# Performance work log

Measured on AMD Instinct MI355X. Metric: run time of the kernel, lower is better.

The kernel has to match this reference:

```python
import jax, jax.numpy as jnp
import numpy as np

B, T, C = 4, 2048, 1024
NH = 16
HD = C // NH

def setup_inputs() -> dict:
    key = jax.random.key(0)
    k1, k2, k3 = jax.random.split(key, 3)
    x = jax.random.normal(k1, (B, T, C), dtype=jnp.float32)
    w_attn = jax.random.normal(k2, (C, 3 * C), dtype=jnp.float32) * (1.0 / np.sqrt(C))
    w_proj = jax.random.normal(k3, (C, C), dtype=jnp.float32) * (1.0 / np.sqrt(C))
    return {"x": x, "w_attn": w_attn, "w_proj": w_proj}

def reference(x, w_attn, w_proj):
    b, t, c = x.shape
    qkv = x @ w_attn  # [B,T,3C]
    q, k, v = jnp.split(qkv, 3, axis=-1)
    # [B,T,C] -> [B,NH,T,HD]
    def heads(a):
        return a.reshape(b, t, NH, HD).transpose(0, 2, 1, 3)
    q, k, v = heads(q), heads(k), heads(v)
    scale = 1.0 / np.sqrt(HD)
    att = jnp.einsum('bhqd,bhkd->bhqk', q, k) * scale  # materialized TxT scores
    causal = jnp.tril(jnp.ones((t, t), dtype=bool))
    att = jnp.where(causal, att, -jnp.inf)
    att = jax.nn.softmax(att, axis=-1)
    y = jnp.einsum('bhqk,bhkd->bhqd', att, v)
    y = y.transpose(0, 2, 1, 3).reshape(b, t, c)
    return y @ w_proj
```

## Files before the change

kernel.cpp:

```cpp
#include <hip/hip_runtime.h>

typedef unsigned short u16;
typedef short bf16x8 __attribute__((ext_vector_type(8)));
typedef float f32x4 __attribute__((ext_vector_type(4)));
typedef float f32x16 __attribute__((ext_vector_type(16)));

#define B_  4
#define T_  2048
#define C_  1024
#define NH_ 16
#define HD_ 64

__device__ __forceinline__ void gload16(const u16* g, u16* lds) {
  __builtin_amdgcn_global_load_lds(
      (const __attribute__((address_space(1))) void*)g,
      (__attribute__((address_space(3))) void*)lds, 16, 0, 0);
}

__device__ __forceinline__ u16 f2bf(float f) {
  union { float f; unsigned u; } x; x.f = f;
  unsigned r = x.u + 0x7fffu + ((x.u >> 16) & 1u);
  return (u16)(r >> 16);
}

__device__ __forceinline__ float max3f(float a, float b, float c) {
  return fmaxf(fmaxf(a, b), c);
}

#define PSWAP(a, b) asm("v_permlane32_swap_b32 %0, %1" : "+v"(a), "+v"(b))

__global__ __launch_bounds__(256) void convert_x(const float* __restrict__ in,
                                                 u16* __restrict__ out) {
  int i = (blockIdx.x * 256 + threadIdx.x) * 8;
  float4 a = *(const float4*)(in + i);
  float4 b = *(const float4*)(in + i + 4);
  u16 t[8] = {f2bf(a.x), f2bf(a.y), f2bf(a.z), f2bf(a.w),
              f2bf(b.x), f2bf(b.y), f2bf(b.z), f2bf(b.w)};
  *(uint4*)(out + i) = *(const uint4*)t;
}

__global__ __launch_bounds__(256) void transpose_w(const float* __restrict__ in,
                                                   u16* __restrict__ out,
                                                   int R, int Cc) {
  int r0 = blockIdx.x * 64, c0 = blockIdx.y * 64;
  __shared__ __attribute__((aligned(16))) u16 tile[64][72];
  int tid = threadIdx.x;
#pragma unroll
  for (int it = 0; it < 4; ++it) {
    int chunk = it * 256 + tid;
    int row = chunk >> 4, c4 = chunk & 15;
    float4 v = *(const float4*)(in + (size_t)(r0 + row) * Cc + c0 + c4 * 4);
    tile[row][c4 * 4 + 0] = f2bf(v.x);
    tile[row][c4 * 4 + 1] = f2bf(v.y);
    tile[row][c4 * 4 + 2] = f2bf(v.z);
    tile[row][c4 * 4 + 3] = f2bf(v.w);
  }
  __syncthreads();
#pragma unroll
  for (int it = 0; it < 2; ++it) {
    int chunk = it * 256 + tid;
    int row = chunk >> 3, c8 = chunk & 7;
    uint4 v; u16* tv = (u16*)&v;
#pragma unroll
    for (int k = 0; k < 8; ++k) tv[k] = tile[c8 * 8 + k][row];
    *(uint4*)(out + (size_t)(c0 + row) * R + r0 + c8 * 8) = v;
  }
}

__device__ __forceinline__ void gemm_bt_tile(const u16* __restrict__ A,
                                             const u16* __restrict__ Bt,
                                             int Kdim, int m0, int n0,
                                             u16* sA, u16* sB, f32x4 acc[4][4]) {
  int tid = threadIdx.x;
  int w = tid >> 6, l = tid & 63, li = l & 15, quad = l >> 4;
  int wm = (w >> 1) * 64, wn = (w & 1) * 64;
  f32x4 zero = {0.f, 0.f, 0.f, 0.f};
#pragma unroll
  for (int i = 0; i < 4; ++i)
#pragma unroll
    for (int j = 0; j < 4; ++j) acc[i][j] = zero;

  for (int k0 = 0; k0 < Kdim; k0 += 32) {
#pragma unroll
    for (int r = 0; r < 2; ++r) {
      int chunk = r * 256 + tid;
      int row = chunk >> 2, c8 = chunk & 3;
      gload16(A  + (size_t)(m0 + row) * Kdim + k0 + c8 * 8, sA + chunk * 8);
      gload16(Bt + (size_t)(n0 + row) * Kdim + k0 + c8 * 8, sB + chunk * 8);
    }
    __syncthreads();
    bf16x8 af[4], bfr[4];
#pragma unroll
    for (int i = 0; i < 4; ++i)
      af[i] = *(const bf16x8*)(sA + (wm + i * 16 + li) * 32 + quad * 8);
#pragma unroll
    for (int j = 0; j < 4; ++j)
      bfr[j] = *(const bf16x8*)(sB + (wn + j * 16 + li) * 32 + quad * 8);
#pragma unroll
    for (int i = 0; i < 4; ++i)
#pragma unroll
      for (int j = 0; j < 4; ++j)
        acc[i][j] = __builtin_amdgcn_mfma_f32_16x16x32_bf16(af[i], bfr[j], acc[i][j], 0, 0, 0);
    __syncthreads();
  }
}

__global__ __launch_bounds__(256) void gemm_qkv(const u16* __restrict__ X,
                                                const u16* __restrict__ WT,
                                                u16* __restrict__ Qb,
                                                u16* __restrict__ Kb,
                                                u16* __restrict__ Vt) {
  __shared__ __attribute__((aligned(16))) u16 sA[128 * 32];
  __shared__ __attribute__((aligned(16))) u16 sB[128 * 32];
  f32x4 acc[4][4];
  int m0 = blockIdx.x * 128, n0 = blockIdx.y * 128;
  gemm_bt_tile(X, WT, C_, m0, n0, sA, sB, acc);

  int tid = threadIdx.x;
  int w = tid >> 6, l = tid & 63, li = l & 15, quad = l >> 4;
  int wm = (w >> 1) * 64, wn = (w & 1) * 64;
#pragma unroll
  for (int i = 0; i < 4; ++i)
#pragma unroll
    for (int j = 0; j < 4; ++j) {
      int n = n0 + wn + j * 16 + li;
      int which = n >> 10, cc = n & (C_ - 1);
      int h = cc >> 6, d = cc & (HD_ - 1);
      int mb = m0 + wm + i * 16 + quad * 4;
      int b = mb >> 11, t0 = mb & (T_ - 1);
      if (which == 2) {
        u16 tv[4] = {f2bf(acc[i][j][0]), f2bf(acc[i][j][1]),
                     f2bf(acc[i][j][2]), f2bf(acc[i][j][3])};
        *(uint2*)(Vt + ((size_t)(b * NH_ + h) * HD_ + d) * T_ + t0) = *(const uint2*)tv;
      } else {
        u16* dst = (which == 0) ? Qb : Kb;
#pragma unroll
        for (int r = 0; r < 4; ++r)
          dst[((size_t)(b * NH_ + h) * T_ + t0 + r) * HD_ + d] = f2bf(acc[i][j][r]);
      }
    }
}

__global__ __launch_bounds__(256) void gemm_proj(const u16* __restrict__ Y,
                                                 const u16* __restrict__ WT,
                                                 float* __restrict__ Out) {
  __shared__ __attribute__((aligned(16))) u16 sA[128 * 32];
  __shared__ __attribute__((aligned(16))) u16 sB[128 * 32];
  f32x4 acc[4][4];
  int m0 = blockIdx.x * 128, n0 = blockIdx.y * 128;
  gemm_bt_tile(Y, WT, C_, m0, n0, sA, sB, acc);

  int tid = threadIdx.x;
  int w = tid >> 6, l = tid & 63, li = l & 15, quad = l >> 4;
  int wm = (w >> 1) * 64, wn = (w & 1) * 64;
#pragma unroll
  for (int i = 0; i < 4; ++i)
#pragma unroll
    for (int j = 0; j < 4; ++j)
#pragma unroll
      for (int r = 0; r < 4; ++r) {
        int m = m0 + wm + i * 16 + quad * 4 + r;
        int n = n0 + wn + j * 16 + li;
        Out[(size_t)m * C_ + n] = acc[i][j][r];
      }
}

__global__ __launch_bounds__(256, 2) void attn_k(const u16* __restrict__ Q,
                                                 const u16* __restrict__ K,
                                                 const u16* __restrict__ Vt,
                                                 u16* __restrict__ Y) {
  int bh = blockIdx.x;
  int qt = 15 - (int)blockIdx.y;
  int tid = threadIdx.x;
  int w = tid >> 6, l = tid & 63;
  int l31 = l & 31, hi = l >> 5;
  int qb = qt * 128 + w * 32;
  int qg = qb + l31;

  __shared__ __attribute__((aligned(16))) u16 sK[2][64 * 64];
  __shared__ __attribute__((aligned(16))) u16 sV[2][64 * 64];

  const u16* kbase = K + (size_t)bh * T_ * HD_;
  const u16* vbase = Vt + (size_t)bh * HD_ * T_;

  bf16x8 qf[4];
  {
    const u16* qp = Q + ((size_t)bh * T_ + qg) * HD_ + hi * 8;
#pragma unroll
    for (int c = 0; c < 4; ++c) qf[c] = *(const bf16x8*)(qp + c * 16);
  }

  f32x16 o[2];
#pragma unroll
  for (int dt = 0; dt < 2; ++dt)
#pragma unroll
    for (int r = 0; r < 16; ++r) o[dt][r] = 0.f;
  float mrow = -1e30f, lsum = 0.f;
  const float csc = 0.125f * 1.44269504088896f;

  int nkv = 2 * qt + 2;

  int koff[2], voff[2], ldst[2];
  {
    int r0 = tid >> 3, c0_ = tid & 7;
#pragma unroll
    for (int rr = 0; rr < 2; ++rr) {
      int row = rr * 32 + r0;
      int cs = (c0_ ^ (row & 7)) * 8;
      koff[rr] = row * HD_ + cs;
      voff[rr] = row * T_ + cs;
      ldst[rr] = (rr * 256 + tid) * 8;
    }
  }
  const u16* kst = kbase;
  const u16* vst = vbase;
#define STAGE(buf)                                        \
  {                                                       \
    gload16(kst + koff[0], sK[buf] + ldst[0]);            \
    gload16(vst + voff[0], sV[buf] + ldst[0]);            \
    gload16(kst + koff[1], sK[buf] + ldst[1]);            \
    gload16(vst + voff[1], sV[buf] + ldst[1]);            \
    kst += 64 * HD_; vst += 64;                           \
  }

  STAGE(0);
  __syncthreads();

  int cur = 0;
  for (int kvt = 0; kvt < nkv; ++kvt) {
    int kv0 = kvt * 64;
    if (kvt + 1 < nkv) STAGE(cur ^ 1);

    bool aq = (kv0 <= qb + 31);
    bool a1 = (kv0 + 32 <= qb + 31);
    if (aq) {
      bf16x8 kf0[4], kf1[4];
#pragma unroll
      for (int c = 0; c < 4; ++c) {
        int row = l31;
        int c16 = (2 * c + hi) ^ (row & 7);
        kf0[c] = *(const bf16x8*)(sK[cur] + row * 64 + c16 * 8);
      }
      if (a1) {
#pragma unroll
        for (int c = 0; c < 4; ++c) {
          int row = 32 + l31;
          int c16 = (2 * c + hi) ^ (row & 7);
          kf1[c] = *(const bf16x8*)(sK[cur] + row * 64 + c16 * 8);
        }
      }

      f32x16 st0, st1;
#pragma unroll
      for (int r = 0; r < 16; ++r) { st0[r] = 0.f; st1[r] = 0.f; }
      __builtin_amdgcn_s_setprio(1);
#pragma unroll
      for (int c = 0; c < 4; ++c)
        st0 = __builtin_amdgcn_mfma_f32_32x32x16_bf16(kf0[c], qf[c], st0, 0, 0, 0);
      if (a1) {
#pragma unroll
        for (int c = 0; c < 4; ++c)
          st1 = __builtin_amdgcn_mfma_f32_32x32x16_bf16(kf1[c], qf[c], st1, 0, 0, 0);
      }
      __builtin_amdgcn_s_setprio(0);

      if (kv0 + 63 > qb) {
#pragma unroll
        for (int r = 0; r < 16; ++r) {
          int kvg = kv0 + (r & 3) + 8 * (r >> 2) + 4 * hi;
          if (kvg > qg) st0[r] = -1e30f;
          if (a1 && kvg + 32 > qg) st1[r] = -1e30f;
        }
      }

      float ml = max3f(st0[0], st0[1], st0[2]);
#pragma unroll
      for (int r = 3; r < 15; r += 2) ml = max3f(ml, st0[r], st0[r + 1]);
      ml = fmaxf(ml, st0[15]);
      if (a1) {
#pragma unroll
        for (int r = 0; r < 16; r += 2) ml = max3f(ml, st1[r], st1[r + 1]);
      }
      float mt = fmaxf(ml, __shfl_xor(ml, 32));
      float g = (mt - mrow) * csc;
      if (!__all(g <= 8.0f)) {
        float mnew = fmaxf(mrow, mt);
        float alpha = exp2f((mrow - mnew) * csc);
        mrow = mnew;
        lsum *= alpha;
#pragma unroll
        for (int r = 0; r < 16; ++r) {
          int qlr = (r & 3) + 8 * (r >> 2) + 4 * hi;
          float ar = __shfl(alpha, qlr);
          o[0][r] *= ar;
          o[1][r] *= ar;
        }
      }

      float mc = mrow * csc;
      float ls = 0.f;
#pragma unroll
      for (int r = 0; r < 16; ++r) {
        float p = exp2f(__builtin_fmaf(st0[r], csc, -mc));
        ls += p; st0[r] = p;
      }
      if (a1) {
#pragma unroll
        for (int r = 0; r < 16; ++r) {
          float p = exp2f(__builtin_fmaf(st1[r], csc, -mc));
          ls += p; st1[r] = p;
        }
      }
      lsum += ls;

      union { unsigned uu[16]; bf16x8 v[4]; } pu;
#pragma unroll
      for (int k = 0; k < 8; ++k)
        asm("v_cvt_pk_bf16_f32 %0, %1, %2"
            : "=v"(pu.uu[k]) : "v"(st0[2 * k]), "v"(st0[2 * k + 1]));
      if (a1) {
#pragma unroll
        for (int k = 0; k < 8; ++k)
          asm("v_cvt_pk_bf16_f32 %0, %1, %2"
              : "=v"(pu.uu[8 + k]) : "v"(st1[2 * k]), "v"(st1[2 * k + 1]));
      }
#pragma unroll
      for (int h2 = 0; h2 < 2; ++h2) {
        PSWAP(pu.uu[4 * h2 + 0], pu.uu[4 * h2 + 2]);
        PSWAP(pu.uu[4 * h2 + 1], pu.uu[4 * h2 + 3]);
      }
      if (a1) {
#pragma unroll
        for (int h2 = 0; h2 < 2; ++h2) {
          PSWAP(pu.uu[8 + 4 * h2 + 0], pu.uu[8 + 4 * h2 + 2]);
          PSWAP(pu.uu[8 + 4 * h2 + 1], pu.uu[8 + 4 * h2 + 3]);
        }
      }

      __builtin_amdgcn_s_setprio(1);
#pragma unroll
      for (int dt = 0; dt < 2; ++dt) {
        bf16x8 vf[4];
#pragma unroll
        for (int c = 0; c < 4; ++c) {
          int row = 32 * dt + l31;
          int c16 = (2 * c + hi) ^ (row & 7);
          vf[c] = *(const bf16x8*)(sV[cur] + row * 64 + c16 * 8);
        }
#pragma unroll
        for (int c = 0; c < 4; ++c) {
          if (c >= 2 && !a1) continue;
          o[dt] = __builtin_amdgcn_mfma_f32_32x32x16_bf16(pu.v[c], vf[c], o[dt], 0, 0, 0);
        }
      }
      __builtin_amdgcn_s_setprio(0);
    }

    __syncthreads();
    cur ^= 1;
  }

  int b = bh >> 4, h = bh & (NH_ - 1);
  float lt = lsum + __shfl_xor(lsum, 32);
  float rv = 1.0f / fmaxf(lt, 1e-20f);
#pragma unroll
  for (int r = 0; r < 16; ++r) {
    int qlr = (r & 3) + 8 * (r >> 2) + 4 * hi;
    float rr = __shfl(rv, qlr);
    int qq = qb + qlr;
    size_t base = ((size_t)b * T_ + qq) * C_ + h * HD_;
    Y[base + l31]      = f2bf(o[0][r] * rr);
    Y[base + 32 + l31] = f2bf(o[1][r] * rr);
  }
#undef STAGE
}

extern "C" void kernel_launch(void* const* d_in, const int* in_sizes, int n_in,
                              void* d_out, int out_size, void* d_ws, size_t ws_size,
                              hipStream_t stream) {
  (void)in_sizes; (void)n_in; (void)out_size; (void)ws_size;
  const float* x      = (const float*)d_in[0];
  const float* w_attn = (const float*)d_in[1];
  const float* w_proj = (const float*)d_in[2];
  float* out = (float*)d_out;

  const size_t NTOK = (size_t)B_ * T_ * C_;
  u16* watT   = (u16*)d_ws;
  u16* wprojT = watT   + (size_t)3 * C_ * C_;
  u16* xbf    = wprojT + (size_t)C_ * C_;
  u16* qb     = xbf  + NTOK;
  u16* kb     = qb   + NTOK;
  u16* vtb    = kb   + NTOK;
  u16* yb     = xbf;

  transpose_w<<<dim3(16, 48), 256, 0, stream>>>(w_attn, watT, C_, 3 * C_);
  transpose_w<<<dim3(16, 16), 256, 0, stream>>>(w_proj, wprojT, C_, C_);
  convert_x<<<dim3(4096), 256, 0, stream>>>(x, xbf);
  gemm_qkv<<<dim3(64, 24), 256, 0, stream>>>(xbf, watT, qb, kb, vtb);
  attn_k<<<dim3(64, 16), 256, 0, stream>>>(qb, kb, vtb, yb);
  gemm_proj<<<dim3(64, 8), 256, 0, stream>>>(yb, wprojT, out);
}
```

Baseline: 251.6 us.

## Triple-buffer GEMM mainloop with swizzled LDS and larger 128x256 tiles

```diff
diff --git a/kernel.cpp b/kernel.cpp
--- a/kernel.cpp
+++ b/kernel.cpp
@@ -67,58 +67,101 @@
   }
 }
 
-__device__ __forceinline__ void gemm_bt_tile(const u16* __restrict__ A,
-                                             const u16* __restrict__ Bt,
-                                             int Kdim, int m0, int n0,
-                                             u16* sA, u16* sB, f32x4 acc[4][4]) {
+__device__ __forceinline__ void gemm_mainloop(const u16* __restrict__ A,
+                                              const u16* __restrict__ Bt,
+                                              int m0, int n0,
+                                              u16* sA0, u16* sA1, u16* sA2,
+                                              u16* sB0, u16* sB1, u16* sB2,
+                                              f32x4 acc[4][4]) {
   int tid = threadIdx.x;
   int w = tid >> 6, l = tid & 63, li = l & 15, quad = l >> 4;
-  int wm = (w >> 1) * 64, wn = (w & 1) * 64;
+  int wr = w >> 2, wc = w & 3;
+
   f32x4 zero = {0.f, 0.f, 0.f, 0.f};
 #pragma unroll
-  for (int i = 0; i < 4; ++i)
-#pragma unroll
-    for (int j = 0; j < 4; ++j) acc[i][j] = zero;
-
-  for (int k0 = 0; k0 < Kdim; k0 += 32) {
-#pragma unroll
-    for (int r = 0; r < 2; ++r) {
-      int chunk = r * 256 + tid;
-      int row = chunk >> 2, c8 = chunk & 3;
-      gload16(A  + (size_t)(m0 + row) * Kdim + k0 + c8 * 8, sA + chunk * 8);
-      gload16(Bt + (size_t)(n0 + row) * Kdim + k0 + c8 * 8, sB + chunk * 8);
+  for (int m = 0; m < 4; ++m)
+#pragma unroll
+    for (int n = 0; n < 4; ++n) acc[m][n] = zero;
+
+  int srow = tid >> 3;
+  int sc = (tid & 7) ^ (srow & 7);
+  const u16* aS0 = A + (size_t)(m0 + srow) * C_ + sc * 8;
+  const u16* aS1 = A + (size_t)(m0 + 64 + srow) * C_ + sc * 8;
+  const u16* bS0 = Bt + (size_t)(n0 + srow) * C_ + sc * 8;
+  const u16* bS1 = Bt + (size_t)(n0 + 64 + srow) * C_ + sc * 8;
+  const u16* bS2 = Bt + (size_t)(n0 + 128 + srow) * C_ + sc * 8;
+  const u16* bS3 = Bt + (size_t)(n0 + 192 + srow) * C_ + sc * 8;
+  int ldOff = tid * 8;
+
+#define STAGE6(sa, sb)                                   \
+  {                                                      \
+    gload16(aS0, (sa) + ldOff);                          \
+    gload16(aS1, (sa) + 4096 + ldOff);                   \
+    gload16(bS0, (sb) + ldOff);                          \
+    gload16(bS1, (sb) + 4096 + ldOff);                   \
+    gload16(bS2, (sb) + 8192 + ldOff);                   \
+    gload16(bS3, (sb) + 12288 + ldOff);                  \
+    aS0 += 64; aS1 += 64;                                \
+    bS0 += 64; bS1 += 64; bS2 += 64; bS3 += 64;          \
+  }
+
+  STAGE6(sA0, sB0);
+  STAGE6(sA1, sB1);
+  asm volatile("s_waitcnt vmcnt(6)" ::: "memory");
+  __builtin_amdgcn_s_barrier();
+
+  u16 *aC = sA0, *aN = sA1, *aSt = sA2;
+  u16 *bC = sB0, *bN = sB1, *bSt = sB2;
+
+  int xr = li & 7;
+  int aRow = (wr * 64 + li) * 64;
+  int bRow = (wc * 64 + li) * 64;
+  int ck0 = (quad ^ xr) * 8;
+  int ck1 = ((4 + quad) ^ xr) * 8;
+
+  for (int kt = 0; kt < 16; ++kt) {
+    STAGE6(aSt, bSt);
+    bf16x8 aF0[4], aF1[4], bF0[4], bF1[4];
+#pragma unroll
+    for (int m = 0; m < 4; ++m) {
+      aF0[m] = *(const bf16x8*)(aC + aRow + m * 1024 + ck0);
+      aF1[m] = *(const bf16x8*)(aC + aRow + m * 1024 + ck1);
     }
-    __syncthreads();
-    bf16x8 af[4], bfr[4];
-#pragma unroll
-    for (int i = 0; i < 4; ++i)
-      af[i] = *(const bf16x8*)(sA + (wm + i * 16 + li) * 32 + quad * 8);
-#pragma unroll
-    for (int j = 0; j < 4; ++j)
-      bfr[j] = *(const bf16x8*)(sB + (wn + j * 16 + li) * 32 + quad * 8);
-#pragma unroll
-    for (int i = 0; i < 4; ++i)
-#pragma unroll
-      for (int j = 0; j < 4; ++j)
-        acc[i][j] = __builtin_amdgcn_mfma_f32_16x16x32_bf16(af[i], bfr[j], acc[i][j], 0, 0, 0);
-    __syncthreads();
-  }
-}
-
-__global__ __launch_bounds__(256) void gemm_qkv(const u16* __restrict__ X,
-                                                const u16* __restrict__ WT,
-                                                u16* __restrict__ Qb,
-                                                u16* __restrict__ Kb,
-                                                u16* __restrict__ Vt) {
-  __shared__ __attribute__((aligned(16))) u16 sA[128 * 32];
-  __shared__ __attribute__((aligned(16))) u16 sB[128 * 32];
+#pragma unroll
+    for (int n = 0; n < 4; ++n) {
+      bF0[n] = *(const bf16x8*)(bC + bRow + n * 1024 + ck0);
+      bF1[n] = *(const bf16x8*)(bC + bRow + n * 1024 + ck1);
+    }
+#pragma unroll
+    for (int m = 0; m < 4; ++m)
+#pragma unroll
+      for (int n = 0; n < 4; ++n) {
+        acc[m][n] = __builtin_amdgcn_mfma_f32_16x16x32_bf16(aF0[m], bF0[n], acc[m][n], 0, 0, 0);
+        acc[m][n] = __builtin_amdgcn_mfma_f32_16x16x32_bf16(aF1[m], bF1[n], acc[m][n], 0, 0, 0);
+      }
+    asm volatile("s_waitcnt vmcnt(6)" ::: "memory");
+    __builtin_amdgcn_s_barrier();
+    u16* t;
+    t = aC; aC = aN; aN = aSt; aSt = t;
+    t = bC; bC = bN; bN = bSt; bSt = t;
+  }
+#undef STAGE6
+}
+
+__global__ __launch_bounds__(512, 2) void gemm_qkv(const u16* __restrict__ X,
+                                                   const u16* __restrict__ WT,
+                                                   u16* __restrict__ Qb,
+                                                   u16* __restrict__ Kb,
+                                                   u16* __restrict__ Vt) {
+  __shared__ __attribute__((aligned(16))) u16 sA[3][128 * 64];
+  __shared__ __attribute__((aligned(16))) u16 sB[3][256 * 64];
   f32x4 acc[4][4];
-  int m0 = blockIdx.x * 128, n0 = blockIdx.y * 128;
-  gemm_bt_tile(X, WT, C_, m0, n0, sA, sB, acc);
+  int m0 = blockIdx.x * 128, n0 = blockIdx.y * 256;
+  gemm_mainloop(X, WT, m0, n0, sA[0], sA[1], sA[2], sB[0], sB[1], sB[2], acc);
 
   int tid = threadIdx.x;
   int w = tid >> 6, l = tid & 63, li = l & 15, quad = l >> 4;
-  int wm = (w >> 1) * 64, wn = (w & 1) * 64;
+  int wm = (w >> 2) * 64, wn = (w & 3) * 64;
 #pragma unroll
   for (int i = 0; i < 4; ++i)
 #pragma unroll
@@ -141,18 +184,18 @@
     }
 }
 
-__global__ __launch_bounds__(256) void gemm_proj(const u16* __restrict__ Y,
-                                                 const u16* __restrict__ WT,
-                                                 float* __restrict__ Out) {
-  __shared__ __attribute__((aligned(16))) u16 sA[128 * 32];
-  __shared__ __attribute__((aligned(16))) u16 sB[128 * 32];
+__global__ __launch_bounds__(512, 2) void gemm_proj(const u16* __restrict__ Y,
+                                                    const u16* __restrict__ WT,
+                                                    float* __restrict__ Out) {
+  __shared__ __attribute__((aligned(16))) u16 sA[3][128 * 64];
+  __shared__ __attribute__((aligned(16))) u16 sB[3][256 * 64];
   f32x4 acc[4][4];
-  int m0 = blockIdx.x * 128, n0 = blockIdx.y * 128;
-  gemm_bt_tile(Y, WT, C_, m0, n0, sA, sB, acc);
+  int m0 = blockIdx.x * 128, n0 = blockIdx.y * 256;
+  gemm_mainloop(Y, WT, m0, n0, sA[0], sA[1], sA[2], sB[0], sB[1], sB[2], acc);
 
   int tid = threadIdx.x;
   int w = tid >> 6, l = tid & 63, li = l & 15, quad = l >> 4;
-  int wm = (w >> 1) * 64, wn = (w & 1) * 64;
+  int wm = (w >> 2) * 64, wn = (w & 3) * 64;
 #pragma unroll
   for (int i = 0; i < 4; ++i)
 #pragma unroll
@@ -396,7 +439,7 @@
   transpose_w<<<dim3(16, 48), 256, 0, stream>>>(w_attn, watT, C_, 3 * C_);
   transpose_w<<<dim3(16, 16), 256, 0, stream>>>(w_proj, wprojT, C_, C_);
   convert_x<<<dim3(4096), 256, 0, stream>>>(x, xbf);
-  gemm_qkv<<<dim3(64, 24), 256, 0, stream>>>(xbf, watT, qb, kb, vtb);
+  gemm_qkv<<<dim3(64, 12), 512, 0, stream>>>(xbf, watT, qb, kb, vtb);
   attn_k<<<dim3(64, 16), 256, 0, stream>>>(qb, kb, vtb, yb);
-  gemm_proj<<<dim3(64, 8), 256, 0, stream>>>(yb, wprojT, out);
-}
+  gemm_proj<<<dim3(64, 4), 512, 0, stream>>>(yb, wprojT, out);
+}
```

Result: no change. 253.1 us (+0.6%).

## Double-buffer GEMM mainloop with BK=64, XOR-swizzled LDS and async prefetch

Applied to the files above, without the earlier changes.

```diff
diff --git a/kernel.cpp b/kernel.cpp
--- a/kernel.cpp
+++ b/kernel.cpp
@@ -67,54 +67,96 @@
   }
 }
 
-__device__ __forceinline__ void gemm_bt_tile(const u16* __restrict__ A,
-                                             const u16* __restrict__ Bt,
-                                             int Kdim, int m0, int n0,
-                                             u16* sA, u16* sB, f32x4 acc[4][4]) {
+__device__ __forceinline__ void gemm_mainloop(const u16* __restrict__ A,
+                                              const u16* __restrict__ Bt,
+                                              int m0, int n0,
+                                              u16* s0, u16* s1,
+                                              f32x4 acc[4][4]) {
   int tid = threadIdx.x;
   int w = tid >> 6, l = tid & 63, li = l & 15, quad = l >> 4;
-  int wm = (w >> 1) * 64, wn = (w & 1) * 64;
+  int wr = w >> 1, wc = w & 1;
+
   f32x4 zero = {0.f, 0.f, 0.f, 0.f};
 #pragma unroll
-  for (int i = 0; i < 4; ++i)
-#pragma unroll
-    for (int j = 0; j < 4; ++j) acc[i][j] = zero;
-
-  for (int k0 = 0; k0 < Kdim; k0 += 32) {
-#pragma unroll
-    for (int r = 0; r < 2; ++r) {
-      int chunk = r * 256 + tid;
-      int row = chunk >> 2, c8 = chunk & 3;
-      gload16(A  + (size_t)(m0 + row) * Kdim + k0 + c8 * 8, sA + chunk * 8);
-      gload16(Bt + (size_t)(n0 + row) * Kdim + k0 + c8 * 8, sB + chunk * 8);
+  for (int m = 0; m < 4; ++m)
+#pragma unroll
+    for (int n = 0; n < 4; ++n) acc[m][n] = zero;
+
+  int srow = tid >> 3;
+  int sc = (tid & 7) ^ (srow & 7);
+  const u16* aS[4];
+  const u16* bS[4];
+#pragma unroll
+  for (int i = 0; i < 4; ++i) {
+    aS[i] = A + (size_t)(m0 + i * 32 + srow) * C_ + sc * 8;
+    bS[i] = Bt + (size_t)(n0 + i * 32 + srow) * C_ + sc * 8;
+  }
+  int ldOff = tid * 8;
+
+#define STAGE8(sbuf)                                      \
+  {                                                       \
+    _Pragma("unroll")                                     \
+    for (int i = 0; i < 4; ++i) {                         \
+      gload16(aS[i], (sbuf) + i * 2048 + ldOff);          \
+      gload16(bS[i], (sbuf) + 8192 + i * 2048 + ldOff);   \
+      aS[i] += 64; bS[i] += 64;                           \
+    }                                                     \
+  }
+
+  int xr = li & 7;
+  int ck0 = (quad ^ xr) * 8;
+  int ck1 = ((4 + quad) ^ xr) * 8;
+  int aRow = (wr * 64 + li) * 64;
+  int bRow = 8192 + (wc * 64 + li) * 64;
+
+  u16* scur = s0;
+  u16* snxt = s1;
+  STAGE8(scur);
+
+  for (int kt = 0; kt < 16; ++kt) {
+    STAGE8(snxt);
+    asm volatile("s_waitcnt vmcnt(8)" ::: "memory");
+    __builtin_amdgcn_s_barrier();
+    asm volatile("" ::: "memory");
+
+    bf16x8 aF0[4], aF1[4], bF0[4], bF1[4];
+#pragma unroll
+    for (int m = 0; m < 4; ++m) {
+      aF0[m] = *(const bf16x8*)(scur + aRow + m * 1024 + ck0);
+      aF1[m] = *(const bf16x8*)(scur + aRow + m * 1024 + ck1);
     }
-    __syncthreads();
-    bf16x8 af[4], bfr[4];
-#pragma unroll
-    for (int i = 0; i < 4; ++i)
-      af[i] = *(const bf16x8*)(sA + (wm + i * 16 + li) * 32 + quad * 8);
-#pragma unroll
-    for (int j = 0; j < 4; ++j)
-      bfr[j] = *(const bf16x8*)(sB + (wn + j * 16 + li) * 32 + quad * 8);
-#pragma unroll
-    for (int i = 0; i < 4; ++i)
-#pragma unroll
-      for (int j = 0; j < 4; ++j)
-        acc[i][j] = __builtin_amdgcn_mfma_f32_16x16x32_bf16(af[i], bfr[j], acc[i][j], 0, 0, 0);
-    __syncthreads();
-  }
-}
-
-__global__ __launch_bounds__(256) void gemm_qkv(const u16* __restrict__ X,
-                                                const u16* __restrict__ WT,
-                                                u16* __restrict__ Qb,
-                                                u16* __restrict__ Kb,
-                                                u16* __restrict__ Vt) {
-  __shared__ __attribute__((aligned(16))) u16 sA[128 * 32];
-  __shared__ __attribute__((aligned(16))) u16 sB[128 * 32];
+#pragma unroll
+    for (int n = 0; n < 4; ++n) {
+      bF0[n] = *(const bf16x8*)(scur + bRow + n * 1024 + ck0);
+      bF1[n] = *(const bf16x8*)(scur + bRow + n * 1024 + ck1);
+    }
+    __builtin_amdgcn_s_setprio(1);
+#pragma unroll
+    for (int m = 0; m < 4; ++m)
+#pragma unroll
+      for (int n = 0; n < 4; ++n) {
+        acc[m][n] = __builtin_amdgcn_mfma_f32_16x16x32_bf16(aF0[m], bF0[n], acc[m][n], 0, 0, 0);
+        acc[m][n] = __builtin_amdgcn_mfma_f32_16x16x32_bf16(aF1[m], bF1[n], acc[m][n], 0, 0, 0);
+      }
+    __builtin_amdgcn_s_setprio(0);
+
+    asm volatile("" ::: "memory");
+    __builtin_amdgcn_s_barrier();
+    asm volatile("" ::: "memory");
+    u16* t = scur; scur = snxt; snxt = t;
+  }
+#undef STAGE8
+}
+
+__global__ __launch_bounds__(256, 2) void gemm_qkv(const u16* __restrict__ X,
+                                                   const u16* __restrict__ WT,
+                                                   u16* __restrict__ Qb,
+                                                   u16* __restrict__ Kb,
+                                                   u16* __restrict__ Vt) {
+  __shared__ __attribute__((aligned(16))) u16 sBuf[2][128 * 64 * 2];
   f32x4 acc[4][4];
   int m0 = blockIdx.x * 128, n0 = blockIdx.y * 128;
-  gemm_bt_tile(X, WT, C_, m0, n0, sA, sB, acc);
+  gemm_mainloop(X, WT, m0, n0, sBuf[0], sBuf[1], acc);
 
   int tid = threadIdx.x;
   int w = tid >> 6, l = tid & 63, li = l & 15, quad = l >> 4;
@@ -141,14 +183,13 @@
     }
 }
 
-__global__ __launch_bounds__(256) void gemm_proj(const u16* __restrict__ Y,
-                                                 const u16* __restrict__ WT,
-                                                 float* __restrict__ Out) {
-  __shared__ __attribute__((aligned(16))) u16 sA[128 * 32];
-  __shared__ __attribute__((aligned(16))) u16 sB[128 * 32];
+__global__ __launch_bounds__(256, 2) void gemm_proj(const u16* __restrict__ Y,
+                                                    const u16* __restrict__ WT,
+                                                    float* __restrict__ Out) {
+  __shared__ __attribute__((aligned(16))) u16 sBuf[2][128 * 64 * 2];
   f32x4 acc[4][4];
   int m0 = blockIdx.x * 128, n0 = blockIdx.y * 128;
-  gemm_bt_tile(Y, WT, C_, m0, n0, sA, sB, acc);
+  gemm_mainloop(Y, WT, m0, n0, sBuf[0], sBuf[1], acc);
 
   int tid = threadIdx.x;
   int w = tid >> 6, l = tid & 63, li = l & 15, quad = l >> 4;
```

Result: faster. 229.2 us (-8.9%).
